# Performance work log

Hardware: AMD Instinct MI355X
Metric: run time of the kernel (lower is better)

The kernel has to match this reference:

```python
import jax, jax.numpy as jnp
import numpy as np

N_AUG = 3
DROPOUT = 0.2
DS_MIN = 0.8
DS_MAX = 1.2
MIXUP_P = 0.3
ALPHA = 0.4
GENE_P = 0.2
INCL_X = False


def _cross_dataset_mixup(key, x, y, ctx):
    """Vectorized same-class / different-dataset mixup.

    Replaces the per-sample Python loop with a [B,B] candidate mask,
    a uniform random pick of the k-th candidate, and a masked blend.
    """
    B = x.shape[0]
    k_sel, k_pick, k_lam, k_coin = jax.random.split(key, 4)
    mix_mask = jax.random.uniform(k_sel, (B,)) < MIXUP_P
    # candidate[i, j] = same label, different context (self excluded since ctx equal)
    cand = (y[None, :] == y[:, None]) & (ctx[None, :] != ctx[:, None])  # [B,B] bool
    counts = cand.sum(axis=1)                                           # [B]
    # uniform pick of the k-th candidate per row
    u = jax.random.uniform(k_pick, (B,))
    kth = jnp.minimum(jnp.floor(u * counts).astype(jnp.int32),
                      jnp.maximum(counts - 1, 0).astype(jnp.int32))
    csum = jnp.cumsum(cand.astype(jnp.int32), axis=1)                   # [B,B]
    j_sel = jnp.argmax(csum > kth[:, None], axis=1)                     # [B]
    lam = jax.random.beta(k_lam, ALPHA, ALPHA, (B,)).astype(x.dtype)
    do_mix = mix_mask & (counts > 0)
    x_mix = lam[:, None] * x + (1.0 - lam[:, None]) * x[j_sel]
    x_new = jnp.where(do_mix[:, None], x_mix, x)
    # 50/50: keep own ctx or take parent's ctx
    coin = jax.random.uniform(k_coin, (B,)) < 0.5
    ctx_new = jnp.where(do_mix & (~coin), ctx[j_sel], ctx)
    return x_new, ctx_new


def _rep(t, repeat):
    # torch: t.repeat(repeat, 1).flatten()
    reps = (repeat,) + (1,) * (t.ndim - 1)
    return jnp.tile(t, reps).reshape(-1)


def setup_inputs() -> dict:
    key = jax.random.key(0)
    kx, kc, ky, kcc, kcat = jax.random.split(key, 5)
    B, D = 2048, 20000
    x = jax.random.normal(kx, (B, D), dtype=jnp.float32)
    ctx = jax.random.randint(kc, (B,), 0, 8)
    y = jax.random.randint(ky, (B,), 0, 50)
    cont_covs = jax.random.normal(kcc, (B, 4), dtype=jnp.float32)
    cat_covs = jax.random.randint(kcat, (B, 2), 0, 10)
    return {"x": x, "ctx": ctx, "y": y, "cont_covs": cont_covs, "cat_covs": cat_covs}


def reference(x, ctx, y, cont_covs, cat_covs):
    B, D = x.shape
    x = x.astype(jnp.float32)
    base_key = jax.random.key(42)
    augmented = []
    ctxs = []
    if INCL_X:
        augmented.append(x)
    for a in range(N_AUG):
        k = jax.random.fold_in(base_key, a)
        k_mix, k_drop, k_scale, k_gmask, k_gscale, k_noise = jax.random.split(k, 6)
        aug, mix_ctx = _cross_dataset_mixup(k_mix, x, y, ctx)
        # dropout: keep where rand > p
        if DROPOUT > 0:
            keep = (jax.random.uniform(k_drop, (B, D)) > DROPOUT).astype(aug.dtype)
            aug = aug * keep
        # per-sample downsample scale in [min, max]
        scale = jax.random.uniform(k_scale, (B, 1)) * (DS_MAX - DS_MIN) + DS_MIN
        aug = aug * scale
        # per-gene random rescale in [0.8, 1.2] on a random subset
        gmask = jax.random.uniform(k_gmask, (D,)) < GENE_P
        gscale = jnp.where(gmask, jax.random.uniform(k_gscale, (D,)) * 0.4 + 0.8, 1.0)
        aug = aug * gscale[None, :]
        # additive gaussian noise, then clamp at zero
        aug = aug + jax.random.normal(k_noise, (B, D)) * 0.01
        augmented.append(jnp.maximum(aug, 0.0))
        ctxs.append(mix_ctx)
    repeat = len(augmented)
    augmented_counts = jnp.concatenate(augmented, axis=0)   # [repeat*B, D]
    augmented_ctxs = jnp.concatenate(ctxs, axis=0).reshape(-1)
    return (augmented_counts,
            augmented_ctxs,
            _rep(y, repeat),
            _rep(cont_covs, repeat),
            _rep(cat_covs, repeat))
```

## Files before the change

kernel.cpp:

```cpp
#include <hip/hip_runtime.h>
#include <cstdint>
#include <cstddef>

#pragma clang fp contract(off)

typedef unsigned int u32;
typedef unsigned long long u64;

__host__ __device__ __forceinline__ u32 rotl32(u32 x, int r) {
  return __builtin_rotateleft32(x, (unsigned)r);
}

__host__ __device__ __forceinline__ void tf2x32(u32 k0, u32 k1, u32 x0, u32 x1,
                                                u32& o0, u32& o1) {
  u32 k2 = k0 ^ k1 ^ 0x1BD11BDAu;
  x0 += k0; x1 += k1;
#define TFR(r) { x0 += x1; x1 = rotl32(x1, r); x1 ^= x0; }
  TFR(13) TFR(15) TFR(26) TFR(6)   x0 += k1; x1 += k2 + 1u;
  TFR(17) TFR(29) TFR(16) TFR(24)  x0 += k2; x1 += k0 + 2u;
  TFR(13) TFR(15) TFR(26) TFR(6)   x0 += k0; x1 += k1 + 3u;
  TFR(17) TFR(29) TFR(16) TFR(24)  x0 += k1; x1 += k2 + 4u;
  TFR(13) TFR(15) TFR(26) TFR(6)   x0 += k2; x1 += k0 + 5u;
#undef TFR
  o0 = x0; o1 = x1;
}

__device__ __forceinline__ u32 bits32(u32 k0, u32 k1, u32 idx) {
  u32 a, b;
  tf2x32(k0, k1, 0u, idx, a, b);
  return a ^ b;
}

__device__ __forceinline__ float u01f(u32 bits) {
  return __uint_as_float((bits >> 9) | 0x3F800000u) - 1.0f;
}

__device__ float erfinv32(float x) {
  float w = -log1pf(-(x * x));
  float p;
  if (w < 5.0f) {
    w = w - 2.5f;
    p = 2.81022636e-08f;
    p = p * w + 3.43273939e-07f;
    p = p * w + -3.5233877e-06f;
    p = p * w + -4.39150654e-06f;
    p = p * w + 0.00021858087f;
    p = p * w + -0.00125372503f;
    p = p * w + -0.00417768164f;
    p = p * w + 0.246640727f;
    p = p * w + 1.50140941f;
  } else {
    w = sqrtf(w) - 3.0f;
    p = -0.000200214257f;
    p = p * w + 0.000100950558f;
    p = p * w + 0.00134934322f;
    p = p * w + -0.00367342844f;
    p = p * w + 0.00573950773f;
    p = p * w + -0.0076224613f;
    p = p * w + 0.00943887047f;
    p = p * w + 1.00167406f;
    p = p * w + 2.83297682f;
  }
  return p * x;
}

__device__ __forceinline__ float normal_from_bits(u32 bits) {
  float f = u01f(bits);
  const float lo = __uint_as_float(0xBF7FFFFFu);
  float u = f * 2.0f + lo;
  u = fmaxf(lo, u);
  return 1.41421356237f * erfinv32(u);
}

__device__ __forceinline__ float noise001(u32 bits) {
  float f01 = u01f(bits);
  const float lo = __uint_as_float(0xBF7FFFFFu);
  float u = __builtin_fmaf(f01, 2.0f, lo);
  u = fmaxf(lo, u);
  float x2m = __builtin_fmaf(-u, u, 1.0f);
  float w = __log2f(x2m) * -0.69314718056f;
  float su = 0.0141421356237f * u;
  float p;
  if (w < 5.0f) {
    w = w - 2.5f;
    p = 2.81022636e-08f;
    p = __builtin_fmaf(p, w, 3.43273939e-07f);
    p = __builtin_fmaf(p, w, -3.5233877e-06f);
    p = __builtin_fmaf(p, w, -4.39150654e-06f);
    p = __builtin_fmaf(p, w, 0.00021858087f);
    p = __builtin_fmaf(p, w, -0.00125372503f);
    p = __builtin_fmaf(p, w, -0.00417768164f);
    p = __builtin_fmaf(p, w, 0.246640727f);
    p = __builtin_fmaf(p, w, 1.50140941f);
  } else {
    w = sqrtf(w) - 3.0f;
    p = -0.000200214257f;
    p = __builtin_fmaf(p, w, 0.000100950558f);
    p = __builtin_fmaf(p, w, 0.00134934322f);
    p = __builtin_fmaf(p, w, -0.00367342844f);
    p = __builtin_fmaf(p, w, 0.00573950773f);
    p = __builtin_fmaf(p, w, -0.0076224613f);
    p = __builtin_fmaf(p, w, 0.00943887047f);
    p = __builtin_fmaf(p, w, 1.00167406f);
    p = __builtin_fmaf(p, w, 2.83297682f);
  }
  return p * su;
}

__device__ float loggamma_alpha04(u32 k0, u32 k1) {
  const float third = (float)(1.0 / 3.0);
  float alpha = 0.4f + 1.0f;
  float d = alpha - third;
  float c = third / sqrtf(d);

  u32 key0, key1, sk0, sk1;
  tf2x32(k0, k1, 0u, 0u, key0, key1);
  tf2x32(k0, k1, 0u, 1u, sk0, sk1);
  float u_boost = u01f(bits32(sk0, sk1, 0u));
  float boost = log1pf(-u_boost) * 2.5f;

  float X, V, U;
  do {
    u32 a0, a1, b0, b1, c0, c1;
    tf2x32(key0, key1, 0u, 0u, a0, a1);
    tf2x32(key0, key1, 0u, 1u, b0, b1);
    tf2x32(key0, key1, 0u, 2u, c0, c1);
    key0 = a0; key1 = a1;
    u32 xk0 = b0, xk1 = b1;
    float x, v;
    do {
      u32 n0, n1, s0, s1;
      tf2x32(xk0, xk1, 0u, 0u, n0, n1);
      tf2x32(xk0, xk1, 0u, 1u, s0, s1);
      x = normal_from_bits(bits32(s0, s1, 0u));
      v = 1.0f + x * c;
      xk0 = n0; xk1 = n1;
    } while (v <= 0.0f);
    X = x * x;
    V = (v * v) * v;
    U = u01f(bits32(c0, c1, 0u));
  } while ((U >= 1.0f - (0.0331f * X) * X) &&
           (logf(U) >= X * 0.5f + d * ((1.0f - V) + logf(V))));

  float lg = logf(d) + logf(V);
  return lg + boost;
}

__device__ float beta_04(u32 la0, u32 la1, u32 lb0, u32 lb1, u32 i) {
  u32 ka0, ka1, kb0, kb1;
  tf2x32(la0, la1, 0u, i, ka0, ka1);
  tf2x32(lb0, lb1, 0u, i, kb0, kb1);
  float lga = loggamma_alpha04(ka0, ka1);
  float lgb = loggamma_alpha04(kb0, kb1);
  float m = fmaxf(lga, lgb);
  float ga = expf(lga - m);
  float gb = expf(lgb - m);
  return ga / (ga + gb);
}

struct RK {
  u32 sel0, sel1, pick0, pick1, la0, la1, lb0, lb1, coin0, coin1;
  u32 drop0, drop1, scl0, scl1, gm0, gm1, gs0, gs1, noi0, noi1;
};
struct AK { RK r[3]; };

__global__ __launch_bounds__(256) void k_meta(
    const int* __restrict__ ctx, const int* __restrict__ y,
    const float* __restrict__ cont, const int* __restrict__ cat,
    AK keys, int B, int ncont, int ncat,
    float* __restrict__ lam_ws, int* __restrict__ jsel_ws,
    int* __restrict__ domix_ws, float* __restrict__ scale_ws,
    float* __restrict__ out,
    unsigned long long o_ctx, unsigned long long o_y,
    unsigned long long o_cont, unsigned long long o_cat) {
  int wv = threadIdx.x >> 6;
  int lane = threadIdx.x & 63;
  int t = blockIdx.x * 4 + wv;
  if (t >= 3 * B) return;
  int a = t / B, i = t - a * B;
  RK rk = keys.r[a];
  int yi = y[i], ci = ctx[i];

  int nch = (B + 63) >> 6;
  int cnt = 0;
  for (int c = 0; c < nch; ++c) {
    int j = (c << 6) + lane;
    bool pred = false;
    if (j < B) pred = (y[j] == yi) && (ctx[j] != ci);
    u64 m = __ballot(pred);
    cnt += __popcll(m);
  }

  float usel = u01f(bits32(rk.sel0, rk.sel1, (u32)i));
  bool mixmask = usel < 0.3f;
  float upick = u01f(bits32(rk.pick0, rk.pick1, (u32)i));
  int kth = min((int)floorf(upick * (float)cnt), max(cnt - 1, 0));

  int jsel = 0, csum = 0;
  for (int c = 0; c < nch; ++c) {
    int j = (c << 6) + lane;
    bool pred = false;
    if (j < B) pred = (y[j] == yi) && (ctx[j] != ci);
    u64 m = __ballot(pred);
    int pc = __popcll(m);
    if (csum + pc > kth) {
      int r = kth - csum;
      for (int z = 0; z < r; ++z) m &= m - 1;
      jsel = (c << 6) + __builtin_ctzll(m);
      break;
    }
    csum += pc;
  }

  float lam = beta_04(rk.la0, rk.la1, rk.lb0, rk.lb1, (u32)i);
  bool domix = mixmask && (cnt > 0);
  bool coin = u01f(bits32(rk.coin0, rk.coin1, (u32)i)) < 0.5f;
  int ctxnew = (domix && !coin) ? ctx[jsel] : ci;
  float uscale = u01f(bits32(rk.scl0, rk.scl1, (u32)i));
  float scale = uscale * 0.4f + 0.8f;

  if (lane == 0) {
    lam_ws[t] = lam;
    jsel_ws[t] = jsel;
    domix_ws[t] = domix ? 1 : 0;
    scale_ws[t] = scale;
    out[o_ctx + (size_t)t] = (float)ctxnew;
    out[o_y + (size_t)t] = (float)yi;
    for (int c2 = 0; c2 < ncont; ++c2)
      out[o_cont + (size_t)t * ncont + c2] = cont[(size_t)i * ncont + c2];
    for (int c2 = 0; c2 < ncat; ++c2)
      out[o_cat + (size_t)t * ncat + c2] = (float)cat[(size_t)i * ncat + c2];
  }
}

__global__ __launch_bounds__(256) void k_gene(AK keys, int D, float* __restrict__ gscale_ws) {
  int t = blockIdx.x * blockDim.x + threadIdx.x;
  if (t >= 3 * D) return;
  int a = t / D, d = t - a * D;
  RK rk = keys.r[a];
  float ug = u01f(bits32(rk.gm0, rk.gm1, (u32)d));
  float us = u01f(bits32(rk.gs0, rk.gs1, (u32)d));
  float gs = us * 0.4f + 0.8f;
  gscale_ws[t] = (ug < 0.2f) ? gs : 1.0f;
}

__global__ __launch_bounds__(256) void k_main(
    const float* __restrict__ x, AK keys, int B, int D,
    const float* __restrict__ lam_ws, const int* __restrict__ jsel_ws,
    const int* __restrict__ domix_ws, const float* __restrict__ scale_ws,
    const float* __restrict__ gscale_ws, float* __restrict__ out) {
  int q = blockIdx.x * blockDim.x + threadIdx.x;
  int d0 = q * 8;
  if (d0 >= D) return;
  int i = blockIdx.y;
  int a = blockIdx.z;
  int t = a * B + i;
  RK rk = keys.r[a];
  float lam = lam_ws[t];
  int jsel = jsel_ws[t];
  int domix = domix_ws[t];
  float scale = scale_ws[t];

  const float4* xip = (const float4*)(x + (size_t)i * D + d0);
  float4 xa = xip[0], xb = xip[1];
  float4 ja_ = xa, jb_ = xb;
  if (domix) {
    const float4* xjp = (const float4*)(x + (size_t)jsel * D + d0);
    ja_ = xjp[0]; jb_ = xjp[1];
  }
  const float4* gp = (const float4*)(gscale_ws + (size_t)a * D + d0);
  float4 ga = gp[0], gb = gp[1];

  float xiv[8] = {xa.x, xa.y, xa.z, xa.w, xb.x, xb.y, xb.z, xb.w};
  float xjv[8] = {ja_.x, ja_.y, ja_.z, ja_.w, jb_.x, jb_.y, jb_.z, jb_.w};
  float gv[8]  = {ga.x, ga.y, ga.z, ga.w, gb.x, gb.y, gb.z, gb.w};
  float oml = 1.0f - lam;
  u32 base = (u32)(i * D + d0);

  float r[8];
#pragma unroll
  for (int e = 0; e < 8; ++e) {
    u32 idx = base + (u32)e;
    u32 bd = bits32(rk.drop0, rk.drop1, idx);
    bool keep = (bd >> 9) > 0x199999u;
    u32 bn = bits32(rk.noi0, rk.noi1, idx);
    float nz = noise001(bn);
    float bse = domix ? __builtin_fmaf(lam, xiv[e], oml * xjv[e]) : xiv[e];
    float v = keep ? bse * (scale * gv[e]) : 0.0f;
    r[e] = fmaxf(v + nz, 0.0f);
  }
  float4 o0; o0.x = r[0]; o0.y = r[1]; o0.z = r[2]; o0.w = r[3];
  float4 o1; o1.x = r[4]; o1.y = r[5]; o1.z = r[6]; o1.w = r[7];
  float4* op = (float4*)(out + (size_t)a * B * D + (size_t)i * D + d0);
  op[0] = o0; op[1] = o1;
}

extern "C" void kernel_launch(void* const* d_in, const int* in_sizes, int n_in,
                              void* d_out, int out_size, void* d_ws, size_t ws_size,
                              hipStream_t stream) {
  const float* x = (const float*)d_in[0];
  const int* ctx = (const int*)d_in[1];
  const int* y = (const int*)d_in[2];
  const float* cont = (const float*)d_in[3];
  const int* cat = (const int*)d_in[4];
  int B = in_sizes[1];
  int D = in_sizes[0] / B;
  int ncont = in_sizes[3] / B;
  int ncat = in_sizes[4] / B;

  AK keys;
  u32 b0 = 0u, b1 = 42u;
  for (int a = 0; a < 3; ++a) {
    u32 k0, k1;
    tf2x32(b0, b1, 0u, (u32)a, k0, k1);
    u32 m0, m1;
    tf2x32(k0, k1, 0u, 0u, m0, m1);
    tf2x32(k0, k1, 0u, 1u, keys.r[a].drop0, keys.r[a].drop1);
    tf2x32(k0, k1, 0u, 2u, keys.r[a].scl0, keys.r[a].scl1);
    tf2x32(k0, k1, 0u, 3u, keys.r[a].gm0, keys.r[a].gm1);
    tf2x32(k0, k1, 0u, 4u, keys.r[a].gs0, keys.r[a].gs1);
    tf2x32(k0, k1, 0u, 5u, keys.r[a].noi0, keys.r[a].noi1);
    tf2x32(m0, m1, 0u, 0u, keys.r[a].sel0, keys.r[a].sel1);
    tf2x32(m0, m1, 0u, 1u, keys.r[a].pick0, keys.r[a].pick1);
    u32 l0, l1;
    tf2x32(m0, m1, 0u, 2u, l0, l1);
    tf2x32(m0, m1, 0u, 3u, keys.r[a].coin0, keys.r[a].coin1);
    tf2x32(l0, l1, 0u, 0u, keys.r[a].la0, keys.r[a].la1);
    tf2x32(l0, l1, 0u, 1u, keys.r[a].lb0, keys.r[a].lb1);
  }

  float* lam_ws = (float*)d_ws;
  int* jsel_ws = (int*)(lam_ws + (size_t)3 * B);
  int* domix_ws = jsel_ws + (size_t)3 * B;
  float* scale_ws = (float*)(domix_ws + (size_t)3 * B);
  float* gscale_ws = scale_ws + (size_t)3 * B;

  float* out = (float*)d_out;
  size_t BD = (size_t)B * D;
  unsigned long long o_ctx = 3ull * BD;
  unsigned long long o_y = o_ctx + 3ull * B;
  unsigned long long o_cont = o_y + 3ull * B;
  unsigned long long o_cat = o_cont + 3ull * (size_t)B * ncont;

  int nwave = 3 * B;
  k_meta<<<(nwave + 3) / 4, 256, 0, stream>>>(
      ctx, y, cont, cat, keys, B, ncont, ncat,
      lam_ws, jsel_ws, domix_ws, scale_ws, out, o_ctx, o_y, o_cont, o_cat);

  int ngene = 3 * D;
  k_gene<<<(ngene + 255) / 256, 256, 0, stream>>>(keys, D, gscale_ws);

  int nq = (D + 7) / 8;
  dim3 grid((nq + 255) / 256, B, 3);
  k_main<<<grid, 256, 0, stream>>>(x, keys, B, D, lam_ws, jsel_ws, domix_ws,
                                   scale_ws, gscale_ws, out);
}
```

Baseline: 952.5 us.

## Fold noise scaling into erfinv polynomial, widen per-thread work, merge setup kernels

Rewrites the noise erfinv evaluation so the polynomial runs directly in log2 space, with the 0.01*sqrt(2) factor and log conversion folded into the coefficients. This removes a multiply per element and the sqrt-domain conversion on the common branch. The dropout test becomes a direct 32-bit compare, and each k_main thread now handles 16 elements instead of 8 to amortise per-row setup. The meta and gene-scale kernels are merged into one launch to save a kernel launch. The refitted coefficients may not match the reference bit-for-bit, and the wider per-thread work raises register pressure.

```diff
diff --git a/kernel.cpp b/kernel.cpp
--- a/kernel.cpp
+++ b/kernel.cpp
@@ -72,39 +72,40 @@
   return 1.41421356237f * erfinv32(u);
 }
 
-__device__ __forceinline__ float noise001(u32 bits) {
+__device__ __forceinline__ float noise_coef(u32 bits, float& u_out) {
   float f01 = u01f(bits);
   const float lo = __uint_as_float(0xBF7FFFFFu);
   float u = __builtin_fmaf(f01, 2.0f, lo);
   u = fmaxf(lo, u);
+  u_out = u;
   float x2m = __builtin_fmaf(-u, u, 1.0f);
-  float w = __log2f(x2m) * -0.69314718056f;
-  float su = 0.0141421356237f * u;
+  float L = __log2f(x2m);
   float p;
-  if (w < 5.0f) {
-    w = w - 2.5f;
-    p = 2.81022636e-08f;
-    p = __builtin_fmaf(p, w, 3.43273939e-07f);
-    p = __builtin_fmaf(p, w, -3.5233877e-06f);
-    p = __builtin_fmaf(p, w, -4.39150654e-06f);
-    p = __builtin_fmaf(p, w, 0.00021858087f);
-    p = __builtin_fmaf(p, w, -0.00125372503f);
-    p = __builtin_fmaf(p, w, -0.00417768164f);
-    p = __builtin_fmaf(p, w, 0.246640727f);
-    p = __builtin_fmaf(p, w, 1.50140941f);
+  if (L > -7.2134752f) {
+    float t = L + 3.6067376f;
+    p = 2.1176800e-11f;
+    p = __builtin_fmaf(p, t, -3.7320220e-10f);
+    p = __builtin_fmaf(p, t, -5.5262215e-09f);
+    p = __builtin_fmaf(p, t, 9.9370327e-09f);
+    p = __builtin_fmaf(p, t, 7.1356898e-07f);
+    p = __builtin_fmaf(p, t, 5.9044800e-06f);
+    p = __builtin_fmaf(p, t, -2.8386004e-05f);
+    p = __builtin_fmaf(p, t, -2.4177128e-03f);
+    p = __builtin_fmaf(p, t, 2.1233136e-02f);
   } else {
-    w = sqrtf(w) - 3.0f;
-    p = -0.000200214257f;
-    p = __builtin_fmaf(p, w, 0.000100950558f);
-    p = __builtin_fmaf(p, w, 0.00134934322f);
-    p = __builtin_fmaf(p, w, -0.00367342844f);
-    p = __builtin_fmaf(p, w, 0.00573950773f);
-    p = __builtin_fmaf(p, w, -0.0076224613f);
-    p = __builtin_fmaf(p, w, 0.00943887047f);
-    p = __builtin_fmaf(p, w, 1.00167406f);
-    p = __builtin_fmaf(p, w, 2.83297682f);
-  }
-  return p * su;
+    float w = L * -0.69314718f;
+    float z = sqrtf(w) - 3.0f;
+    p = -2.8314686e-06f;
+    p = __builtin_fmaf(p, z, 1.4276572e-06f);
+    p = __builtin_fmaf(p, z, 1.9082658e-05f);
+    p = __builtin_fmaf(p, z, -5.1950125e-05f);
+    p = __builtin_fmaf(p, z, 8.1168923e-05f);
+    p = __builtin_fmaf(p, z, -1.0779792e-04f);
+    p = __builtin_fmaf(p, z, 1.3348577e-04f);
+    p = __builtin_fmaf(p, z, 1.4165810e-02f);
+    p = __builtin_fmaf(p, z, 4.0064342e-02f);
+  }
+  return p;
 }
 
 __device__ float loggamma_alpha04(u32 k0, u32 k1) {
@@ -164,15 +165,26 @@
 };
 struct AK { RK r[3]; };
 
-__global__ __launch_bounds__(256) void k_meta(
+__global__ __launch_bounds__(256) void k_small(
     const int* __restrict__ ctx, const int* __restrict__ y,
     const float* __restrict__ cont, const int* __restrict__ cat,
-    AK keys, int B, int ncont, int ncat,
+    AK keys, int B, int D, int ncont, int ncat, int mb,
     float* __restrict__ lam_ws, int* __restrict__ jsel_ws,
     int* __restrict__ domix_ws, float* __restrict__ scale_ws,
-    float* __restrict__ out,
+    float* __restrict__ gscale_ws, float* __restrict__ out,
     unsigned long long o_ctx, unsigned long long o_y,
     unsigned long long o_cont, unsigned long long o_cat) {
+  if ((int)blockIdx.x >= mb) {
+    int t = ((int)blockIdx.x - mb) * 256 + threadIdx.x;
+    if (t >= 3 * D) return;
+    int a = t / D, d = t - a * D;
+    RK rk = keys.r[a];
+    float ug = u01f(bits32(rk.gm0, rk.gm1, (u32)d));
+    float us = u01f(bits32(rk.gs0, rk.gs1, (u32)d));
+    float gs = us * 0.4f + 0.8f;
+    gscale_ws[t] = (ug < 0.2f) ? gs : 1.0f;
+    return;
+  }
   int wv = threadIdx.x >> 6;
   int lane = threadIdx.x & 63;
   int t = blockIdx.x * 4 + wv;
@@ -233,24 +245,13 @@
   }
 }
 
-__global__ __launch_bounds__(256) void k_gene(AK keys, int D, float* __restrict__ gscale_ws) {
-  int t = blockIdx.x * blockDim.x + threadIdx.x;
-  if (t >= 3 * D) return;
-  int a = t / D, d = t - a * D;
-  RK rk = keys.r[a];
-  float ug = u01f(bits32(rk.gm0, rk.gm1, (u32)d));
-  float us = u01f(bits32(rk.gs0, rk.gs1, (u32)d));
-  float gs = us * 0.4f + 0.8f;
-  gscale_ws[t] = (ug < 0.2f) ? gs : 1.0f;
-}
-
 __global__ __launch_bounds__(256) void k_main(
     const float* __restrict__ x, AK keys, int B, int D,
     const float* __restrict__ lam_ws, const int* __restrict__ jsel_ws,
     const int* __restrict__ domix_ws, const float* __restrict__ scale_ws,
     const float* __restrict__ gscale_ws, float* __restrict__ out) {
   int q = blockIdx.x * blockDim.x + threadIdx.x;
-  int d0 = q * 8;
+  int d0 = q * 16;
   if (d0 >= D) return;
   int i = blockIdx.y;
   int a = blockIdx.z;
@@ -262,37 +263,46 @@
   float scale = scale_ws[t];
 
   const float4* xip = (const float4*)(x + (size_t)i * D + d0);
-  float4 xa = xip[0], xb = xip[1];
-  float4 ja_ = xa, jb_ = xb;
+  float4 xi4[4] = {xip[0], xip[1], xip[2], xip[3]};
+  float4 xj4[4] = {xi4[0], xi4[1], xi4[2], xi4[3]};
   if (domix) {
     const float4* xjp = (const float4*)(x + (size_t)jsel * D + d0);
-    ja_ = xjp[0]; jb_ = xjp[1];
+    xj4[0] = xjp[0]; xj4[1] = xjp[1]; xj4[2] = xjp[2]; xj4[3] = xjp[3];
   }
   const float4* gp = (const float4*)(gscale_ws + (size_t)a * D + d0);
-  float4 ga = gp[0], gb = gp[1];
-
-  float xiv[8] = {xa.x, xa.y, xa.z, xa.w, xb.x, xb.y, xb.z, xb.w};
-  float xjv[8] = {ja_.x, ja_.y, ja_.z, ja_.w, jb_.x, jb_.y, jb_.z, jb_.w};
-  float gv[8]  = {ga.x, ga.y, ga.z, ga.w, gb.x, gb.y, gb.z, gb.w};
+  float4 g4[4] = {gp[0], gp[1], gp[2], gp[3]};
+
   float oml = 1.0f - lam;
   u32 base = (u32)(i * D + d0);
 
-  float r[8];
+  float r[16];
 #pragma unroll
-  for (int e = 0; e < 8; ++e) {
-    u32 idx = base + (u32)e;
-    u32 bd = bits32(rk.drop0, rk.drop1, idx);
-    bool keep = (bd >> 9) > 0x199999u;
-    u32 bn = bits32(rk.noi0, rk.noi1, idx);
-    float nz = noise001(bn);
-    float bse = domix ? __builtin_fmaf(lam, xiv[e], oml * xjv[e]) : xiv[e];
-    float v = keep ? bse * (scale * gv[e]) : 0.0f;
-    r[e] = fmaxf(v + nz, 0.0f);
-  }
-  float4 o0; o0.x = r[0]; o0.y = r[1]; o0.z = r[2]; o0.w = r[3];
-  float4 o1; o1.x = r[4]; o1.y = r[5]; o1.z = r[6]; o1.w = r[7];
+  for (int v4 = 0; v4 < 4; ++v4) {
+    const float* xiv = (const float*)&xi4[v4];
+    const float* xjv = (const float*)&xj4[v4];
+    const float* gvv = (const float*)&g4[v4];
+#pragma unroll
+    for (int e = 0; e < 4; ++e) {
+      int ee = v4 * 4 + e;
+      u32 idx = base + (u32)ee;
+      u32 bd = bits32(rk.drop0, rk.drop1, idx);
+      bool keep = bd >= 0x33333400u;
+      u32 bn = bits32(rk.noi0, rk.noi1, idx);
+      float u;
+      float pc = noise_coef(bn, u);
+      float bse = domix ? __builtin_fmaf(lam, xiv[e], oml * xjv[e]) : xiv[e];
+      float v = keep ? bse * (scale * gvv[e]) : 0.0f;
+      r[ee] = fmaxf(__builtin_fmaf(pc, u, v), 0.0f);
+    }
+  }
   float4* op = (float4*)(out + (size_t)a * B * D + (size_t)i * D + d0);
-  op[0] = o0; op[1] = o1;
+#pragma unroll
+  for (int v4 = 0; v4 < 4; ++v4) {
+    float4 o;
+    o.x = r[v4 * 4 + 0]; o.y = r[v4 * 4 + 1];
+    o.z = r[v4 * 4 + 2]; o.w = r[v4 * 4 + 3];
+    op[v4] = o;
+  }
 }
 
 extern "C" void kernel_launch(void* const* d_in, const int* in_sizes, int n_in,
@@ -342,15 +352,14 @@
   unsigned long long o_cont = o_y + 3ull * B;
   unsigned long long o_cat = o_cont + 3ull * (size_t)B * ncont;
 
-  int nwave = 3 * B;
-  k_meta<<<(nwave + 3) / 4, 256, 0, stream>>>(
-      ctx, y, cont, cat, keys, B, ncont, ncat,
-      lam_ws, jsel_ws, domix_ws, scale_ws, out, o_ctx, o_y, o_cont, o_cat);
-
-  int ngene = 3 * D;
-  k_gene<<<(ngene + 255) / 256, 256, 0, stream>>>(keys, D, gscale_ws);
-
-  int nq = (D + 7) / 8;
+  int mb = (3 * B + 3) / 4;
+  int gb = (3 * D + 255) / 256;
+  k_small<<<mb + gb, 256, 0, stream>>>(
+      ctx, y, cont, cat, keys, B, D, ncont, ncat, mb,
+      lam_ws, jsel_ws, domix_ws, scale_ws, gscale_ws, out,
+      o_ctx, o_y, o_cont, o_cat);
+
+  int nq = (D + 15) / 16;
   dim3 grid((nq + 255) / 256, B, 3);
   k_main<<<grid, 256, 0, stream>>>(x, keys, B, D, lam_ws, jsel_ws, domix_ws,
                                    scale_ws, gscale_ws, out);
```

Result: no change. 964.5 us (+1.3%).
